# Optimization experiments

Measured on AMD Instinct MI355X. Metric: run time of the kernel, lower is better.

## Reference

```python
import jax, jax.numpy as jnp
import numpy as np

B, N, TOKEN_DIM = 8, 1024, 768
H, D = 12, 64  # n_heads, head_dim


def setup_inputs() -> dict:
    key = jax.random.key(0)
    k1, k2, k3, k4 = jax.random.split(key, 4)
    x = jax.random.normal(k1, (B, N, TOKEN_DIM), dtype=jnp.float32)
    # nn.Linear(token_dim, 3*H*D, bias=False); store as (in, out)
    W_qkv = jax.random.normal(k2, (TOKEN_DIM, 3 * H * D), dtype=jnp.float32) * (TOKEN_DIM ** -0.5)
    # nn.Linear(H*D, token_dim) with bias
    W_out = jax.random.normal(k3, (H * D, TOKEN_DIM), dtype=jnp.float32) * ((H * D) ** -0.5)
    b_out = jax.random.normal(k4, (TOKEN_DIM,), dtype=jnp.float32) * 0.01
    return {"x": x, "W_qkv": W_qkv, "W_out": W_out, "b_out": b_out}


def reference(x, W_qkv, W_out, b_out):
    b, n, _ = x.shape
    qkv = x @ W_qkv                              # (B, N, 3*H*D)
    # Faithful to original: reshape directly to (B, 3, H, N, D)
    qkv = qkv.reshape(b, 3, H, n, D)
    q, k, v = qkv[:, 0], qkv[:, 1], qkv[:, 2]    # each (B, H, N, D)
    scale = D ** -0.5
    scores = jnp.einsum('bhnd,bhmd->bhnm', q, k) * scale
    probs = jax.nn.softmax(scores, axis=-1)
    attn = jnp.einsum('bhnm,bhmd->bhnd', probs, v)  # (B, H, N, D)
    attn = attn.transpose(0, 2, 1, 3).reshape(b, n, H * D)
    out = attn @ W_out + b_out                    # dropout p=0.0 is identity
    return out
```

## Files before the change

### kernel.cpp

```cpp
#include <hip/hip_runtime.h>
#include <math.h>

static constexpr int NB   = 8;
static constexpr int SEQ  = 1024;
static constexpr int TD   = 768;
static constexpr int NH   = 12;
static constexpr int HD   = 64;
static constexpr int QKVC = 3 * NH * HD;

static constexpr size_t BATCH_ELEMS = (size_t)SEQ * QKVC;
static constexpr size_t THIRD_ELEMS = (size_t)NH * SEQ * HD;
static constexpr size_t HEAD_ELEMS  = (size_t)SEQ * HD;

typedef __bf16 bf16x8 __attribute__((ext_vector_type(8)));
typedef __bf16 bf16x4 __attribute__((ext_vector_type(4)));
typedef float  f32x4  __attribute__((ext_vector_type(4)));

#define MFMA16(a, b, c) __builtin_amdgcn_mfma_f32_16x16x32_bf16((a), (b), (c), 0, 0, 0)

static constexpr float SCL2E = 0.18033688011112042f;

__device__ __forceinline__ void gload_lds16(const void* g, void* l) {
  __builtin_amdgcn_global_load_lds(
      (const __attribute__((address_space(1))) unsigned int*)g,
      (__attribute__((address_space(3))) unsigned int*)l, 16, 0, 0);
}

__global__ __launch_bounds__(256) void prep(const float* __restrict__ x,
                                            const float* __restrict__ Wq,
                                            const float* __restrict__ Wo,
                                            __bf16* __restrict__ xb,
                                            __bf16* __restrict__ wqt,
                                            __bf16* __restrict__ wot) {
  const int blk = blockIdx.x;
  const int tid = threadIdx.x;
  if (blk < 6144) {
    int i = blk * 256 + tid;
    float4 v = ((const float4*)x)[i];
    bf16x4 o;
    o[0] = (__bf16)v.x; o[1] = (__bf16)v.y; o[2] = (__bf16)v.z; o[3] = (__bf16)v.w;
    ((bf16x4*)xb)[i] = o;
    return;
  }
  __shared__ float T[32 * 33];
  const float* W;
  __bf16* Wt;
  int K, N, k0, n0;
  if (blk < 6144 + 1728) {
    int bidx = blk - 6144;
    W = Wq; Wt = wqt; K = TD; N = QKVC;
    k0 = (bidx / 72) * 32; n0 = (bidx % 72) * 32;
  } else {
    int bidx = blk - 7872;
    W = Wo; Wt = wot; K = TD; N = TD;
    k0 = (bidx / 24) * 32; n0 = (bidx % 24) * 32;
  }
#pragma unroll
  for (int i = 0; i < 4; ++i) {
    int idx = tid + i * 256;
    int kk = idx >> 5, nn = idx & 31;
    T[kk * 33 + nn] = W[(size_t)(k0 + kk) * N + n0 + nn];
  }
  __syncthreads();
#pragma unroll
  for (int i = 0; i < 4; ++i) {
    int idx = tid + i * 256;
    int nn = idx >> 5, kk = idx & 31;
    Wt[(size_t)(n0 + nn) * K + k0 + kk] = (__bf16)T[kk * 33 + nn];
  }
}

__global__ __launch_bounds__(256) void vtrans(const __bf16* __restrict__ qkvb,
                                              __bf16* __restrict__ vtb) {
  const int nt = blockIdx.x;
  const int h = blockIdx.y;
  const int b = blockIdx.z;
  __shared__ __bf16 T[128 * 72];
  const int tid = threadIdx.x;
  const int n0 = nt * 128;
  const __bf16* Vb = qkvb + (size_t)b * BATCH_ELEMS + 2 * THIRD_ELEMS + (size_t)h * HEAD_ELEMS;
#pragma unroll
  for (int i = 0; i < 4; ++i) {
    int ch = tid + i * 256;
    int row = ch >> 3, c8 = ch & 7;
    *(bf16x8*)&T[row * 72 + c8 * 8] = *(const bf16x8*)&Vb[(size_t)(n0 + row) * HD + c8 * 8];
  }
  __syncthreads();
#pragma unroll
  for (int i = 0; i < 4; ++i) {
    int ch = tid + i * 256;
    int d = ch >> 4, n8 = ch & 15;
    bf16x8 v;
#pragma unroll
    for (int jj = 0; jj < 8; ++jj) {
      int j = (jj + n8) & 7;
      v[j] = T[(n8 * 8 + j) * 72 + d];
    }
    *(bf16x8*)&vtb[((size_t)((b * NH + h) * HD) + d) * SEQ + n0 + n8 * 8] = v;
  }
}

template <int MODE, int BM, int BN>
__global__ __launch_bounds__(256) void gemm_mfma(const __bf16* __restrict__ A,
                                                 const __bf16* __restrict__ Bt,
                                                 const float* __restrict__ bias,
                                                 void* __restrict__ C,
                                                 int M, int N, int K) {
  constexpr int MI = BM / 32;
  constexpr int NJ = BN / 32;
  __shared__ __bf16 As[2][BM * 32];
  __shared__ __bf16 Bs[2][BN * 32];
  const int tid = threadIdx.x;
  const int lane = tid & 63;
  const int wid = tid >> 6;
  const int wr = wid >> 1, wc = wid & 1;
  const int r = lane & 15, g = lane >> 4;
  const size_t bm = (size_t)blockIdx.y * BM;
  const size_t bn = (size_t)blockIdx.x * BN;

  const int srow = lane >> 2;
  const int scol = (lane & 3) * 8;

  auto stage = [&](int buf, int k0) {
#pragma unroll
    for (int j = 0; j < BM / 64; ++j) {
      const int rowbase = wid * (BM / 4) + j * 16;
      gload_lds16(&A[(bm + rowbase + srow) * K + k0 + scol], &As[buf][rowbase * 32]);
    }
#pragma unroll
    for (int j = 0; j < BN / 64; ++j) {
      const int rowbase = wid * (BN / 4) + j * 16;
      gload_lds16(&Bt[(bn + rowbase + srow) * K + k0 + scol], &Bs[buf][rowbase * 32]);
    }
  };

  f32x4 acc[MI][NJ];
#pragma unroll
  for (int mi = 0; mi < MI; ++mi)
#pragma unroll
    for (int nj = 0; nj < NJ; ++nj) acc[mi][nj] = (f32x4){0.f, 0.f, 0.f, 0.f};

  stage(0, 0);
  __syncthreads();

  int cur = 0;
  for (int k0 = 0; k0 < K; k0 += 32) {
    if (k0 + 32 < K) stage(cur ^ 1, k0 + 32);
    bf16x8 af[MI], bf[NJ];
#pragma unroll
    for (int mi = 0; mi < MI; ++mi)
      af[mi] = *(const bf16x8*)&As[cur][(wr * (BM / 2) + mi * 16 + r) * 32 + g * 8];
#pragma unroll
    for (int nj = 0; nj < NJ; ++nj)
      bf[nj] = *(const bf16x8*)&Bs[cur][(wc * (BN / 2) + nj * 16 + r) * 32 + g * 8];
#pragma unroll
    for (int mi = 0; mi < MI; ++mi)
#pragma unroll
      for (int nj = 0; nj < NJ; ++nj)
        acc[mi][nj] = MFMA16(af[mi], bf[nj], acc[mi][nj]);
    __syncthreads();
    cur ^= 1;
  }

  const int orow0 = g * 4;
  const int ocol = r;
#pragma unroll
  for (int mi = 0; mi < MI; ++mi)
#pragma unroll
    for (int nj = 0; nj < NJ; ++nj)
#pragma unroll
      for (int reg = 0; reg < 4; ++reg) {
        size_t rrow = bm + wr * (BM / 2) + mi * 16 + orow0 + reg;
        size_t ccol = bn + wc * (BN / 2) + nj * 16 + ocol;
        float v = acc[mi][nj][reg];
        if (MODE == 1) {
          int fwb = ((int)(rrow & (SEQ - 1))) * QKVC + (int)ccol;
          float vv = (fwb < (int)THIRD_ELEMS) ? v * SCL2E : v;
          ((__bf16*)C)[rrow * N + ccol] = (__bf16)vv;
        } else {
          ((float*)C)[rrow * N + ccol] = v + bias[ccol];
        }
      }
}

__global__ __launch_bounds__(256) void attn_mfma(const __bf16* __restrict__ qkvb,
                                                 const __bf16* __restrict__ vtb,
                                                 __bf16* __restrict__ attn2b) {
  const int d = blockIdx.x;
  const int qt = (d >> 3) & 7;
  const int hb = (d >> 6) * 8 + (d & 7);
  const int b = hb / NH, h = hb % NH;

  const int tid = threadIdx.x;
  const int lane = tid & 63;
  const int w = tid >> 6;
  const int c = lane & 15, g = lane >> 4;

  __shared__ __bf16 KsF[2][4096];
  __shared__ __bf16 VsF[2][4096];

  const __bf16* Qb = qkvb + (size_t)b * BATCH_ELEMS + (size_t)h * HEAD_ELEMS;
  const __bf16* Kb = Qb + THIRD_ELEMS;
  const __bf16* Vtb = vtb + (size_t)((b * NH + h) * HD) * SEQ;

  const __bf16* kS[2];
  const __bf16* vS[2];
  int ldsOff[2];
#pragma unroll
  for (int i = 0; i < 2; ++i) {
    const int t2f = i * 4 + w;
    const int t = t2f >> 1, f = t2f & 1;
    const int krow = ((t >> 1) << 5) | ((c >> 2) << 3) | ((t & 1) << 2) | (c & 3);
    kS[i] = Kb + krow * HD + f * 32 + g * 8;
    const int db = t2f >> 1, kk = t2f & 1;
    vS[i] = Vtb + (db * 16 + c) * SEQ + kk * 32 + g * 8;
    ldsOff[i] = t2f * 512;
  }

  bf16x8 qf[2][2];
#pragma unroll
  for (int s = 0; s < 2; ++s) {
    const int q0s = qt * 128 + s * 64 + w * 16;
#pragma unroll
    for (int f = 0; f < 2; ++f)
      qf[s][f] = *(const bf16x8*)&Qb[(size_t)(q0s + c) * HD + f * 32 + g * 8];
  }

  f32x4 Oa[2][4];
#pragma unroll
  for (int s = 0; s < 2; ++s)
#pragma unroll
    for (int db = 0; db < 4; ++db) Oa[s][db] = (f32x4){0.f, 0.f, 0.f, 0.f};
  float lpart[2] = {0.f, 0.f};

#pragma unroll
  for (int i = 0; i < 2; ++i) {
    gload_lds16(kS[i], &KsF[0][ldsOff[i]]);
    gload_lds16(vS[i], &VsF[0][ldsOff[i]]);
    kS[i] += 64 * HD;
    vS[i] += 64;
  }
  __syncthreads();

  int cur = 0;
  for (int it = 0; it < SEQ / 64; ++it) {
    if (it < SEQ / 64 - 1) {
      const int nxt = cur ^ 1;
#pragma unroll
      for (int i = 0; i < 2; ++i) {
        gload_lds16(kS[i], &KsF[nxt][ldsOff[i]]);
        gload_lds16(vS[i], &VsF[nxt][ldsOff[i]]);
        kS[i] += 64 * HD;
        vS[i] += 64;
      }
    }

    f32x4 sa[2][4];
#pragma unroll
    for (int s = 0; s < 2; ++s)
#pragma unroll
      for (int t = 0; t < 4; ++t) sa[s][t] = (f32x4){0.f, 0.f, 0.f, 0.f};
#pragma unroll
    for (int t = 0; t < 4; ++t)
#pragma unroll
      for (int f = 0; f < 2; ++f) {
        bf16x8 kf = *(const bf16x8*)&KsF[cur][(t * 2 + f) * 512 + lane * 8];
        sa[0][t] = MFMA16(kf, qf[0][f], sa[0][t]);
        sa[1][t] = MFMA16(kf, qf[1][f], sa[1][t]);
      }

    bf16x8 pb[2][2];
#pragma unroll
    for (int s = 0; s < 2; ++s) {
      float p[4][4];
      float lp = 0.f;
#pragma unroll
      for (int t = 0; t < 4; ++t)
#pragma unroll
        for (int reg = 0; reg < 4; ++reg) {
          float pv = __builtin_exp2f(sa[s][t][reg]);
          p[t][reg] = pv;
          lp += pv;
        }
      lpart[s] += lp;
#pragma unroll
      for (int kk = 0; kk < 2; ++kk)
#pragma unroll
        for (int i = 0; i < 4; ++i) {
          pb[s][kk][i] = (__bf16)p[2 * kk][i];
          pb[s][kk][4 + i] = (__bf16)p[2 * kk + 1][i];
        }
    }

#pragma unroll
    for (int db = 0; db < 4; ++db)
#pragma unroll
      for (int kk = 0; kk < 2; ++kk) {
        bf16x8 vf = *(const bf16x8*)&VsF[cur][(db * 2 + kk) * 512 + lane * 8];
        Oa[0][db] = MFMA16(vf, pb[0][kk], Oa[0][db]);
        Oa[1][db] = MFMA16(vf, pb[1][kk], Oa[1][db]);
      }

    __syncthreads();
    cur ^= 1;
  }

#pragma unroll
  for (int s = 0; s < 2; ++s) {
    float lrow = lpart[s];
    lrow += __shfl_xor(lrow, 16);
    lrow += __shfl_xor(lrow, 32);
    const float inv = 1.0f / lrow;
    const size_t rowq = (size_t)(b * SEQ) + qt * 128 + s * 64 + w * 16 + c;
#pragma unroll
    for (int db = 0; db < 4; ++db) {
      bf16x4 o;
#pragma unroll
      for (int reg = 0; reg < 4; ++reg) o[reg] = (__bf16)(Oa[s][db][reg] * inv);
      *(bf16x4*)&attn2b[rowq * TD + h * HD + db * 16 + g * 4] = o;
    }
  }
}

extern "C" void kernel_launch(void* const* d_in, const int* in_sizes, int n_in,
                              void* d_out, int out_size, void* d_ws,
                              size_t ws_size, hipStream_t stream) {
  const float* x = (const float*)d_in[0];
  const float* W_qkv = (const float*)d_in[1];
  const float* W_out = (const float*)d_in[2];
  const float* b_out = (const float*)d_in[3];
  float* out = (float*)d_out;

  __bf16* xb = (__bf16*)d_ws;
  __bf16* wqkvt = xb + (size_t)NB * SEQ * TD;
  __bf16* woutt = wqkvt + (size_t)QKVC * TD;
  __bf16* qkvb = woutt + (size_t)TD * TD;
  __bf16* vtb = qkvb + (size_t)NB * SEQ * QKVC;
  __bf16* attn2b = vtb + (size_t)NB * NH * HD * SEQ;

  prep<<<dim3(8448), 256, 0, stream>>>(x, W_qkv, W_out, xb, wqkvt, woutt);

  gemm_mfma<1, 128, 192><<<dim3(QKVC / 192, NB * SEQ / 128), 256, 0, stream>>>(
      xb, wqkvt, nullptr, qkvb, NB * SEQ, QKVC, TD);

  vtrans<<<dim3(SEQ / 128, NH, NB), 256, 0, stream>>>(qkvb, vtb);

  attn_mfma<<<dim3(SEQ / 128 * NH * NB), 256, 0, stream>>>(qkvb, vtb, attn2b);

  gemm_mfma<0, 64, 128><<<dim3(TD / 128, NB * SEQ / 64), 256, 0, stream>>>(
      attn2b, woutt, b_out, out, NB * SEQ, TD, TD);
}
```

Before: 136.7 us.

## Software-pipeline attention loop with triple-buffered K/V and overlapped QK/softmax/PV

Restructures the attention main loop into a three-stage software pipeline. QK^T for tile i+1 is issued alongside the softmax and PV for tile i, with K/V staged into a third LDS buffer, so MFMA work can overlap the exp2 math and the global-to-LDS loads. This raises LDS usage from 32KB to 48KB per block and keeps a second set of score registers live, which may cut occupancy. The loop is now explicitly unrolled by two and runs once per iteration.

```diff
diff --git a/kernel.cpp b/kernel.cpp
--- a/kernel.cpp
+++ b/kernel.cpp
@@ -196,12 +196,14 @@
   const int w = tid >> 6;
   const int c = lane & 15, g = lane >> 4;
 
-  __shared__ __bf16 KsF[2][4096];
-  __shared__ __bf16 VsF[2][4096];
+  __shared__ __bf16 KsF[3][4096];
+  __shared__ __bf16 VsF[3][4096];
 
   const __bf16* Qb = qkvb + (size_t)b * BATCH_ELEMS + (size_t)h * HEAD_ELEMS;
   const __bf16* Kb = Qb + THIRD_ELEMS;
   const __bf16* Vtb = vtb + (size_t)((b * NH + h) * HD) * SEQ;
+
+  const f32x4 ZERO4 = {0.f, 0.f, 0.f, 0.f};
 
   const __bf16* kS[2];
   const __bf16* vS[2];
@@ -230,46 +232,34 @@
 #pragma unroll
   for (int s = 0; s < 2; ++s)
 #pragma unroll
-    for (int db = 0; db < 4; ++db) Oa[s][db] = (f32x4){0.f, 0.f, 0.f, 0.f};
+    for (int db = 0; db < 4; ++db) Oa[s][db] = ZERO4;
   float lpart[2] = {0.f, 0.f};
-
-#pragma unroll
-  for (int i = 0; i < 2; ++i) {
-    gload_lds16(kS[i], &KsF[0][ldsOff[i]]);
-    gload_lds16(vS[i], &VsF[0][ldsOff[i]]);
-    kS[i] += 64 * HD;
-    vS[i] += 64;
-  }
-  __syncthreads();
-
-  int cur = 0;
-  for (int it = 0; it < SEQ / 64; ++it) {
-    if (it < SEQ / 64 - 1) {
-      const int nxt = cur ^ 1;
-#pragma unroll
-      for (int i = 0; i < 2; ++i) {
-        gload_lds16(kS[i], &KsF[nxt][ldsOff[i]]);
-        gload_lds16(vS[i], &VsF[nxt][ldsOff[i]]);
-        kS[i] += 64 * HD;
-        vS[i] += 64;
-      }
-    }
-
-    f32x4 sa[2][4];
-#pragma unroll
-    for (int s = 0; s < 2; ++s)
-#pragma unroll
-      for (int t = 0; t < 4; ++t) sa[s][t] = (f32x4){0.f, 0.f, 0.f, 0.f};
-#pragma unroll
-    for (int t = 0; t < 4; ++t)
-#pragma unroll
-      for (int f = 0; f < 2; ++f) {
-        bf16x8 kf = *(const bf16x8*)&KsF[cur][(t * 2 + f) * 512 + lane * 8];
-        sa[0][t] = MFMA16(kf, qf[0][f], sa[0][t]);
-        sa[1][t] = MFMA16(kf, qf[1][f], sa[1][t]);
-      }
-
-    bf16x8 pb[2][2];
+  bf16x8 pb[2][2];
+
+  auto stageTo = [&](int m) {
+#pragma unroll
+    for (int i = 0; i < 2; ++i) {
+      gload_lds16(kS[i], &KsF[m][ldsOff[i]]);
+      gload_lds16(vS[i], &VsF[m][ldsOff[i]]);
+      kS[i] += 64 * HD;
+      vS[i] += 64;
+    }
+  };
+
+  auto qk = [&](f32x4 (&sa)[2][4], int m) {
+    const __bf16* kb = &KsF[m][lane * 8];
+#pragma unroll
+    for (int t = 0; t < 4; ++t) {
+      bf16x8 kf0 = *(const bf16x8*)(kb + (t * 2 + 0) * 512);
+      bf16x8 kf1 = *(const bf16x8*)(kb + (t * 2 + 1) * 512);
+      sa[0][t] = MFMA16(kf0, qf[0][0], ZERO4);
+      sa[1][t] = MFMA16(kf0, qf[1][0], ZERO4);
+      sa[0][t] = MFMA16(kf1, qf[0][1], sa[0][t]);
+      sa[1][t] = MFMA16(kf1, qf[1][1], sa[1][t]);
+    }
+  };
+
+  auto smax = [&](f32x4 (&sa)[2][4]) {
 #pragma unroll
     for (int s = 0; s < 2; ++s) {
       float p[4][4];
@@ -291,19 +281,47 @@
           pb[s][kk][4 + i] = (__bf16)p[2 * kk + 1][i];
         }
     }
-
+  };
+
+  auto pv = [&](int m) {
+    const __bf16* vb = &VsF[m][lane * 8];
 #pragma unroll
     for (int db = 0; db < 4; ++db)
 #pragma unroll
       for (int kk = 0; kk < 2; ++kk) {
-        bf16x8 vf = *(const bf16x8*)&VsF[cur][(db * 2 + kk) * 512 + lane * 8];
+        bf16x8 vf = *(const bf16x8*)(vb + (db * 2 + kk) * 512);
         Oa[0][db] = MFMA16(vf, pb[0][kk], Oa[0][db]);
         Oa[1][db] = MFMA16(vf, pb[1][kk], Oa[1][db]);
       }
-
+  };
+
+  int mpv = 0, mqk = 1, mst = 2;
+
+  auto step = [&](f32x4 (&cur)[2][4], f32x4 (&nxt)[2][4], bool doStage) {
     __syncthreads();
-    cur ^= 1;
-  }
+    if (doStage) stageTo(mst);
+    qk(nxt, mqk);
+    smax(cur);
+    pv(mpv);
+    int t = mpv; mpv = mqk; mqk = mst; mst = t;
+  };
+
+  f32x4 saA[2][4], saB[2][4];
+
+  stageTo(0);
+  __syncthreads();
+  qk(saA, 0);
+  stageTo(1);
+
+#pragma unroll 1
+  for (int ii = 0; ii < 7; ++ii) {
+    step(saA, saB, true);
+    step(saB, saA, true);
+  }
+  step(saA, saB, false);
+
+  smax(saB);
+  pv(mpv);
 
 #pragma unroll
   for (int s = 0; s < 2; ++s) {
```

New measurement: 146.3 us. 7.0% more time.
